# Kernel tuning notes

Measured on AMD Instinct MI355X. Metric: run time of the kernel, lower is better.

The kernel has to match this reference:

```python
import jax, jax.numpy as jnp
import numpy as np

B, N, OBS, H, A = 1024, 64, 128, 256, 16
NH = 4
HD = H // NH


def _linear_params(key, fan_in, fan_out):
    k1, k2 = jax.random.split(key)
    bound = 1.0 / np.sqrt(fan_in)
    W = jax.random.uniform(k1, (fan_out, fan_in), jnp.float32, -bound, bound)
    b = jax.random.uniform(k2, (fan_out,), jnp.float32, -bound, bound)
    return W, b


def setup_inputs() -> dict:
    key = jax.random.key(0)
    ks = jax.random.split(key, 10)
    obs = jax.random.normal(ks[0], (B, N, OBS), jnp.float32)
    adj = jax.random.randint(ks[1], (B, N, N), 0, 2).astype(jnp.float32)
    # guarantee every row has at least one neighbor (self-loop) so softmax is finite
    adj = jnp.maximum(adj, jnp.eye(N, dtype=jnp.float32)[None])
    W1, b1 = _linear_params(ks[2], OBS, H)
    W2, b2 = _linear_params(ks[3], H, H)
    Wq, bq = _linear_params(ks[4], H, H)
    Wk, bk = _linear_params(ks[5], H, H)
    Wv, bv = _linear_params(ks[6], H, H)
    Wo, bo = _linear_params(ks[7], H, H)
    Wc, bc = _linear_params(ks[8], H, H)
    W3, b3 = _linear_params(ks[9], H, A)
    return dict(obs=obs, adj=adj, W1=W1, b1=b1, W2=W2, b2=b2,
                Wq=Wq, bq=bq, Wk=Wk, bk=bk, Wv=Wv, bv=bv,
                Wo=Wo, bo=bo, Wc=Wc, bc=bc, W3=W3, b3=b3)


def reference(obs, adj, W1, b1, W2, b2, Wq, bq, Wk, bk, Wv, bv, Wo, bo, Wc, bc, W3, b3):
    lin = lambda x, W, b: jnp.einsum('bnd,od->bno', x, W) + b
    x = jax.nn.relu(lin(obs, W1, b1))
    x = jax.nn.relu(lin(x, W2, b2))
    # multi-head attention with adjacency mask
    def heads(t):  # [B,N,H] -> [B,NH,N,HD]
        return t.reshape(B, N, NH, HD).transpose(0, 2, 1, 3)
    q = heads(lin(x, Wq, bq))
    k = heads(lin(x, Wk, bk))
    v = heads(lin(x, Wv, bv))
    scores = jnp.einsum('bhqd,bhkd->bhqk', q, k) / np.sqrt(HD).astype(np.float32)
    scores = jnp.where(adj[:, None] == 0, -jnp.inf, scores)
    attn = jax.nn.softmax(scores, axis=-1)
    out = jnp.einsum('bhqk,bhkd->bhqd', attn, v)
    out = out.transpose(0, 2, 1, 3).reshape(B, N, H)
    x = lin(out, Wo, bo)
    # communication: adj @ fc(x)
    x = jnp.einsum('bnm,bmh->bnh', adj, lin(x, Wc, bc))
    return lin(x, W3, b3)
```

## Files before the change

### kernel.cpp

```cpp
#include <hip/hip_runtime.h>
#include <stdint.h>

typedef unsigned short u16;
typedef unsigned long long u64;
typedef __attribute__((ext_vector_type(8))) short short8;
typedef __attribute__((ext_vector_type(4))) float f32x4;

#define MFMA16 __builtin_amdgcn_mfma_f32_16x16x32_bf16

#define MTOT 65536

__device__ __forceinline__ u16 f2bf(float f) {
  union { float f; uint32_t u; } v; v.f = f;
  uint32_t r = v.u + 0x7FFFu + ((v.u >> 16) & 1u);
  return (u16)(r >> 16);
}

union U8 { short8 v; u16 u[8]; };
union U4 { u64 v; u16 u[4]; };

__device__ __forceinline__ void cp16(const void* g, void* l) {
  __builtin_amdgcn_global_load_lds(
      (const __attribute__((address_space(1))) void*)g,
      (__attribute__((address_space(3))) void*)l, 16, 0, 0);
}

__device__ __forceinline__ int swz(int row) { return ((row >> 1) & 3) << 4; }

__global__ __launch_bounds__(256) void k_l1(
    const float* __restrict__ Wc, const float* __restrict__ Wo,
    const float* __restrict__ bo, const float* __restrict__ bc,
    float* __restrict__ M1, float* __restrict__ bv,
    const float* __restrict__ W1, const float* __restrict__ W2,
    const float* __restrict__ Wq, const float* __restrict__ Wk,
    u16* o1, u16* o2, u16* oq, u16* ok) {
  const int bid = blockIdx.x, tid = threadIdx.x;
  if (bid < 256) {
    __shared__ float wcr[256];
    __shared__ float red[4];
    const int j = bid, d = tid;
    wcr[d] = Wc[j * 256 + d];
    __syncthreads();
    float acc = 0.f;
    for (int i = 0; i < 256; i++) acc += wcr[i] * Wo[i * 256 + d];
    M1[j * 256 + d] = acc;
    float p = wcr[d] * bo[d];
    for (int off = 32; off >= 1; off >>= 1) p += __shfl_xor(p, off);
    if ((d & 63) == 0) red[d >> 6] = p;
    __syncthreads();
    if (d == 0) bv[j] = bc[j] + red[0] + red[1] + red[2] + red[3];
  } else {
    int off8 = (bid - 256) * 256 + tid;
    const float* src; u16* dst;
    if      (off8 <  4096) { src = W1; dst = o1; }
    else if (off8 < 12288) { src = W2; dst = o2; off8 -= 4096; }
    else if (off8 < 20480) { src = Wq; dst = oq; off8 -= 12288; }
    else                   { src = Wk; dst = ok; off8 -= 20480; }
    const int e = off8 * 8;
    f32x4 a = *(const f32x4*)(src + e);
    f32x4 b = *(const f32x4*)(src + e + 4);
    U8 pk;
#pragma unroll
    for (int j = 0; j < 4; j++) { pk.u[j] = f2bf(a[j]); pk.u[4 + j] = f2bf(b[j]); }
    *(short8*)(dst + e) = pk.v;
  }
}

template<int K, bool AF32>
__device__ __forceinline__ void gemm_full2(
    const void* __restrict__ Ain, const u16* __restrict__ W,
    const float* __restrict__ bias, u16* __restrict__ C,
    const int m0, const bool relu, char* smem) {
  const int tid = threadIdx.x;
  const int lane = tid & 63, wid = tid >> 6;
  const int wr = wid >> 1, wc = wid & 1;
  const int ro = lane & 15, hi = lane >> 4;

  f32x4 acc0[4][4], acc1[4][4];
#pragma unroll
  for (int m = 0; m < 4; m++)
#pragma unroll
    for (int n = 0; n < 4; n++) {
      acc0[m][n] = (f32x4){0.f, 0.f, 0.f, 0.f};
      acc1[m][n] = (f32x4){0.f, 0.f, 0.f, 0.f};
    }

  auto stage = [&](int buf, int k0) {
    char* Ax = smem + buf * 24576;
    char* Bx = Ax + 8192;
    if (AF32) {
      const float* Af = (const float*)Ain;
#pragma unroll
      for (int it = 0; it < 2; it++) {
        const int e = (tid + it * 256) * 8;
        const int r = e >> 5, c = e & 31;
        const float* s = Af + (size_t)(m0 + r) * K + k0 + c;
        f32x4 a = *(const f32x4*)s, b = *(const f32x4*)(s + 4);
        U8 pk;
#pragma unroll
        for (int j = 0; j < 4; j++) { pk.u[j] = f2bf(a[j]); pk.u[4 + j] = f2bf(b[j]); }
        *(short8*)(Ax + ((r * 64 + c * 2) ^ swz(r))) = pk.v;
      }
    } else {
      const u16* Ab = (const u16*)Ain;
#pragma unroll
      for (int i = 0; i < 2; i++) {
        const int boff = i * 4096 + wid * 1024;
        const int t = boff + lane * 16;
        const int row = t >> 6;
        const int cb = (t & 63) ^ swz(row);
        cp16(Ab + (size_t)(m0 + row) * K + k0 + (cb >> 1), Ax + boff);
      }
    }
#pragma unroll
    for (int i = 0; i < 4; i++) {
      const int boff = i * 4096 + wid * 1024;
      const int t = boff + lane * 16;
      const int row = t >> 6;
      const int cb = (t & 63) ^ swz(row);
      cp16(W + (size_t)row * K + k0 + (cb >> 1), Bx + boff);
    }
  };

  auto compute = [&](int buf) {
    char* Ax = smem + buf * 24576;
    char* Bx = Ax + 8192;
    short8 af[4], fb0[4], fb1[4];
#pragma unroll
    for (int m = 0; m < 4; m++) {
      const int row = wr * 64 + m * 16 + ro;
      af[m] = *(const short8*)(Ax + ((row * 64 + hi * 16) ^ swz(row)));
    }
#pragma unroll
    for (int n = 0; n < 4; n++) {
      const int r0 = wc * 64 + n * 16 + ro;
      fb0[n] = *(const short8*)(Bx + ((r0 * 64 + hi * 16) ^ swz(r0)));
      const int r1 = 128 + r0;
      fb1[n] = *(const short8*)(Bx + ((r1 * 64 + hi * 16) ^ swz(r1)));
    }
    __builtin_amdgcn_s_setprio(1);
#pragma unroll
    for (int m = 0; m < 4; m++)
#pragma unroll
      for (int n = 0; n < 4; n++) {
        acc0[m][n] = MFMA16(af[m], fb0[n], acc0[m][n], 0, 0, 0);
        acc1[m][n] = MFMA16(af[m], fb1[n], acc1[m][n], 0, 0, 0);
      }
    __builtin_amdgcn_s_setprio(0);
  };

  constexpr int NT = K / 32;
  if (AF32) {
    stage(0, 0);
    __syncthreads();
    int cur = 0;
    for (int k0 = 32; k0 < K; k0 += 32) {
      stage(cur ^ 1, k0);
      compute(cur);
      __syncthreads();
      cur ^= 1;
    }
    compute(cur);
    __syncthreads();
  } else {
    stage(0, 0);
    stage(1, 32);
#pragma unroll
    for (int t = 0; t < NT; ++t) {
      if (t == NT - 1) asm volatile("s_waitcnt vmcnt(0)" ::: "memory");
      else             asm volatile("s_waitcnt vmcnt(6)" ::: "memory");
      asm volatile("s_barrier" ::: "memory");
      compute(t & 1);
      asm volatile("s_barrier" ::: "memory");
      if (t + 2 < NT) stage(t & 1, (t + 2) * 32);
    }
  }

  u16 (*Cs)[136] = (u16(*)[136])smem;
  auto ep = [&](f32x4 (&acc)[4][4], const int n0) {
#pragma unroll
    for (int half = 0; half < 2; half++) {
      if (wr == half) {
#pragma unroll
        for (int n = 0; n < 4; n++) {
          const int col = wc * 64 + n * 16 + ro;
          const float bb = bias[n0 + col];
#pragma unroll
          for (int m = 0; m < 4; m++)
#pragma unroll
            for (int j = 0; j < 4; j++) {
              float val = acc[m][n][j] + bb;
              if (relu) val = fmaxf(val, 0.f);
              Cs[m * 16 + hi * 4 + j][col] = f2bf(val);
            }
        }
      }
      __syncthreads();
      for (int i = tid; i < 64 * 16; i += 256) {
        const int r = i >> 4, c = (i & 15) << 3;
        *(short8*)(C + (size_t)(m0 + half * 64 + r) * 256 + n0 + c) = *(short8*)&Cs[r][c];
      }
      __syncthreads();
    }
  };
  ep(acc0, 0);
  ep(acc1, 128);
}

__global__ __launch_bounds__(256, 2) void k_gemm1_prep2(
    const float* __restrict__ obs, const u16* __restrict__ W1b,
    const float* __restrict__ b1, u16* __restrict__ x1,
    const float* __restrict__ W3, const float* __restrict__ M1,
    const float* __restrict__ bvchain, const float* __restrict__ bvw,
    float* __restrict__ Wzf, float* __restrict__ bz) {
  __shared__ char smem[49152];
  if (blockIdx.x < 512) {
    gemm_full2<128, true>(obs, W1b, b1, x1, (int)blockIdx.x * 128, true, smem);
    return;
  }
  float* w3r = (float*)smem;
  float* red = (float*)(smem + 1024);
  const int a = blockIdx.x - 512, d = threadIdx.x;
  w3r[d] = W3[a * 256 + d];
  __syncthreads();
  float acc = 0.f;
  for (int j = 0; j < 256; j++) acc += w3r[j] * M1[j * 256 + d];
  Wzf[a * 256 + d] = acc;
  float p = w3r[d] * bvchain[d] + acc * bvw[d];
  for (int off = 32; off >= 1; off >>= 1) p += __shfl_xor(p, off);
  if ((d & 63) == 0) red[d >> 6] = p;
  __syncthreads();
  if (d == 0) bz[a] = red[0] + red[1] + red[2] + red[3];
}

__global__ __launch_bounds__(256, 2) void k_x2_prep3(
    const u16* __restrict__ x1, const u16* __restrict__ W2b,
    const float* __restrict__ b2, u16* __restrict__ x2,
    const float* __restrict__ Wzf, const float* __restrict__ Wv,
    u16* __restrict__ G) {
  __shared__ char smem[49152];
  if (blockIdx.x < 512) {
    gemm_full2<256, false>(x1, W2b, b2, x2, (int)blockIdx.x * 128, true, smem);
    return;
  }
  const int g = blockIdx.x - 512, d2 = threadIdx.x;
  const int h = g >> 4, a = g & 15;
  float* wzr = (float*)smem;
  if (d2 < 64) wzr[d2] = Wzf[a * 256 + h * 64 + d2];
  __syncthreads();
  float acc = 0.f;
#pragma unroll 8
  for (int d = 0; d < 64; d++) acc += wzr[d] * Wv[(size_t)(h * 64 + d) * 256 + d2];
  G[g * 256 + d2] = f2bf(acc);
}

__global__ __launch_bounds__(256, 2) void k_qk_gemmv(
    const u16* __restrict__ x2,
    const u16* __restrict__ Wqb, const float* __restrict__ bq, u16* __restrict__ Qg,
    const u16* __restrict__ Wkb, const float* __restrict__ bk, u16* __restrict__ Kg,
    const u16* __restrict__ G, u16* __restrict__ Vzt) {
  __shared__ char smem[49152];
  const int bid = blockIdx.x;
  if (bid < 1024) {
    const int q = bid >> 4, r = bid & 15;
    const int mt = q * 8 + (r & 7);
    const int sub = r >> 3;
    gemm_full2<256, false>(x2, sub ? Wkb : Wqb, sub ? bk : bq, sub ? Kg : Qg,
                           mt * 128, false, smem);
    return;
  }
  const int tid = threadIdx.x;
  const int lane = tid & 63, w = tid >> 6;
  const int ro = lane & 15, hi = lane >> 4;
  const int m0 = (bid - 1024) * 128;

  f32x4 acc[2][4];
#pragma unroll
  for (int m = 0; m < 2; m++)
#pragma unroll
    for (int n = 0; n < 4; n++) acc[m][n] = (f32x4){0.f, 0.f, 0.f, 0.f};

  auto stage = [&](int buf, int k0) {
    char* Ax = smem + buf * 12288;
    char* Bx = Ax + 8192;
#pragma unroll
    for (int i = 0; i < 2; i++) {
      const int boff = i * 4096 + w * 1024;
      const int t = boff + lane * 16;
      const int row = t >> 6;
      const int cb = (t & 63) ^ swz(row);
      cp16(x2 + (size_t)(m0 + row) * 256 + k0 + (cb >> 1), Ax + boff);
    }
    {
      const int boff = w * 1024;
      const int t = boff + lane * 16;
      const int row = t >> 6;
      const int cb = (t & 63) ^ swz(row);
      cp16(G + (size_t)row * 256 + k0 + (cb >> 1), Bx + boff);
    }
  };
  auto compute = [&](int buf) {
    char* Ax = smem + buf * 12288;
    char* Bx = Ax + 8192;
    short8 af[2], fb[4];
#pragma unroll
    for (int m = 0; m < 2; m++) {
      const int row = w * 32 + m * 16 + ro;
      af[m] = *(const short8*)(Ax + ((row * 64 + hi * 16) ^ swz(row)));
    }
#pragma unroll
    for (int n = 0; n < 4; n++) {
      const int row = n * 16 + ro;
      fb[n] = *(const short8*)(Bx + ((row * 64 + hi * 16) ^ swz(row)));
    }
    __builtin_amdgcn_s_setprio(1);
#pragma unroll
    for (int m = 0; m < 2; m++)
#pragma unroll
      for (int n = 0; n < 4; n++)
        acc[m][n] = MFMA16(af[m], fb[n], acc[m][n], 0, 0, 0);
    __builtin_amdgcn_s_setprio(0);
  };

  stage(0, 0);
  stage(1, 32);
#pragma unroll
  for (int t = 0; t < 8; ++t) {
    if (t == 7) asm volatile("s_waitcnt vmcnt(0)" ::: "memory");
    else        asm volatile("s_waitcnt vmcnt(3)" ::: "memory");
    asm volatile("s_barrier" ::: "memory");
    compute(t & 1);
    asm volatile("s_barrier" ::: "memory");
    if (t + 2 < 8) stage(t & 1, (t + 2) * 32);
  }

#pragma unroll
  for (int m = 0; m < 2; m++) {
    const int rbase = w * 32 + m * 16;
    const int bidx = (m0 >> 6) + (rbase >> 6);
    const int ke = (rbase + hi * 4) & 63;
#pragma unroll
    for (int n = 0; n < 4; n++) {
      const int c = n * 16 + ro;
      U4 pk;
#pragma unroll
      for (int j = 0; j < 4; j++) pk.u[j] = f2bf(acc[m][n][j]);
      *(u64*)(Vzt + (size_t)bidx * 4096 + (size_t)c * 64 + ke) = pk.v;
    }
  }
}

__global__ __launch_bounds__(256, 2) void attn_fused(
    const u16* __restrict__ Qg, const u16* __restrict__ Kg,
    const u16* __restrict__ Vzt, const float* __restrict__ adj,
    const float* __restrict__ bz, const float* __restrict__ b3,
    float* __restrict__ out) {
  __shared__ u16 Ps[4][64][72];
  __shared__ float Zs[4][64][16];
  __shared__ u64 adjm[64];
  __shared__ u16 chunk[64][4];

  const int b = blockIdx.x, tid = threadIdx.x;
  const int lane = tid & 63, w = tid >> 6;
  const int ro = lane & 15, hi = lane >> 4;
  const int hc = w * 64;
  const size_t base = (size_t)b * 64 * 256;

  short8 kb[4][2];
#pragma unroll
  for (int n = 0; n < 4; n++)
#pragma unroll
    for (int ks = 0; ks < 2; ks++)
      kb[n][ks] = *(const short8*)(Kg + base + (size_t)(n * 16 + ro) * 256 + hc + ks * 32 + hi * 8);

  {
    const int q = tid >> 2, qa = tid & 3;
    const float* ar = adj + ((size_t)b * 64 + q) * 64 + qa * 16;
    f32x4 a0 = *(const f32x4*)(ar);
    f32x4 a1 = *(const f32x4*)(ar + 4);
    f32x4 a2 = *(const f32x4*)(ar + 8);
    f32x4 a3 = *(const f32x4*)(ar + 12);
    unsigned m16 = 0;
#pragma unroll
    for (int i = 0; i < 4; i++) {
      m16 |= (unsigned)(a0[i] != 0.f) << i;
      m16 |= (unsigned)(a1[i] != 0.f) << (4 + i);
      m16 |= (unsigned)(a2[i] != 0.f) << (8 + i);
      m16 |= (unsigned)(a3[i] != 0.f) << (12 + i);
    }
    chunk[q][qa] = (u16)m16;
  }

  f32x4 s[4][4];
#pragma unroll
  for (int m = 0; m < 4; m++) {
    short8 af[2];
#pragma unroll
    for (int ks = 0; ks < 2; ks++)
      af[ks] = *(const short8*)(Qg + base + (size_t)(m * 16 + ro) * 256 + hc + ks * 32 + hi * 8);
#pragma unroll
    for (int n = 0; n < 4; n++) s[m][n] = (f32x4){0.f, 0.f, 0.f, 0.f};
#pragma unroll
    for (int ks = 0; ks < 2; ks++)
#pragma unroll
      for (int n = 0; n < 4; n++)
        s[m][n] = MFMA16(af[ks], kb[n][ks], s[m][n], 0, 0, 0);
  }

  short8 vz[2];
#pragma unroll
  for (int ks = 0; ks < 2; ks++)
    vz[ks] = *(const short8*)(Vzt + (size_t)b * 4096 + (size_t)(hc / 4 + ro) * 64 + ks * 32 + hi * 8);

  __syncthreads();
  if (tid < 64)
    adjm[tid] = (u64)chunk[tid][0] | ((u64)chunk[tid][1] << 16) |
                ((u64)chunk[tid][2] << 32) | ((u64)chunk[tid][3] << 48);
  __syncthreads();

#pragma unroll
  for (int m = 0; m < 4; m++) {
#pragma unroll
    for (int j = 0; j < 4; j++) {
      const int q = m * 16 + hi * 4 + j;
      const u64 msk = adjm[q];
      float sv[4], ev[4];
      float mx = -3.0e38f;
#pragma unroll
      for (int n = 0; n < 4; n++) {
        const bool on = (msk >> (n * 16 + ro)) & 1ull;
        sv[n] = on ? s[m][n][j] * 0.125f : -3.0e38f;
        mx = fmaxf(mx, sv[n]);
      }
      mx = fmaxf(mx, __shfl_xor(mx, 1));
      mx = fmaxf(mx, __shfl_xor(mx, 2));
      mx = fmaxf(mx, __shfl_xor(mx, 4));
      mx = fmaxf(mx, __shfl_xor(mx, 8));
      float sum = 0.f;
#pragma unroll
      for (int n = 0; n < 4; n++) {
        ev[n] = (sv[n] > -1.0e37f) ? __expf(sv[n] - mx) : 0.f;
        sum += ev[n];
      }
      sum += __shfl_xor(sum, 1);
      sum += __shfl_xor(sum, 2);
      sum += __shfl_xor(sum, 4);
      sum += __shfl_xor(sum, 8);
      const float inv = 1.0f / sum;
#pragma unroll
      for (int n = 0; n < 4; n++)
        Ps[w][q][n * 16 + ro] = f2bf(ev[n] * inv);
    }
  }

#pragma unroll
  for (int m = 0; m < 4; m++) {
    short8 pa[2];
    pa[0] = *(const short8*)&Ps[w][m * 16 + ro][hi * 8];
    pa[1] = *(const short8*)&Ps[w][m * 16 + ro][32 + hi * 8];
    f32x4 oz = (f32x4){0.f, 0.f, 0.f, 0.f};
#pragma unroll
    for (int ks = 0; ks < 2; ks++)
      oz = MFMA16(pa[ks], vz[ks], oz, 0, 0, 0);
#pragma unroll
    for (int j = 0; j < 4; j++)
      Zs[w][m * 16 + hi * 4 + j][ro] = oz[j];
  }
  __syncthreads();

  for (int i = tid; i < 1024; i += 256) {
    const int r = i >> 4, a = i & 15;
    Zs[0][r][a] += Zs[1][r][a] + Zs[2][r][a] + Zs[3][r][a];
  }
  __syncthreads();

  {
    const int n = tid >> 2, a4 = (tid & 3) << 2;
    const u64 msk = adjm[n];
    const float deg = (float)__popcll(msk);
    float a0 = 0.f, a1 = 0.f, a2 = 0.f, a3 = 0.f;
#pragma unroll 8
    for (int m = 0; m < 64; m++) {
      const float wv = (float)((msk >> m) & 1ull);
      f32x4 z = *(const f32x4*)&Zs[0][m][a4];
      a0 += wv * z[0]; a1 += wv * z[1]; a2 += wv * z[2]; a3 += wv * z[3];
    }
    f32x4 r;
    r[0] = a0 + b3[a4 + 0] + deg * bz[a4 + 0];
    r[1] = a1 + b3[a4 + 1] + deg * bz[a4 + 1];
    r[2] = a2 + b3[a4 + 2] + deg * bz[a4 + 2];
    r[3] = a3 + b3[a4 + 3] + deg * bz[a4 + 3];
    *(f32x4*)(out + ((size_t)b * 64 + n) * 16 + a4) = r;
  }
}

extern "C" void kernel_launch(void* const* d_in, const int* in_sizes, int n_in,
                              void* d_out, int out_size, void* d_ws, size_t ws_size,
                              hipStream_t stream) {
  const float* obs = (const float*)d_in[0];
  const float* adj = (const float*)d_in[1];
  const float* W1  = (const float*)d_in[2];
  const float* b1  = (const float*)d_in[3];
  const float* W2  = (const float*)d_in[4];
  const float* b2  = (const float*)d_in[5];
  const float* Wq  = (const float*)d_in[6];
  const float* bq  = (const float*)d_in[7];
  const float* Wk  = (const float*)d_in[8];
  const float* bk  = (const float*)d_in[9];
  const float* Wv  = (const float*)d_in[10];
  const float* bvw = (const float*)d_in[11];
  const float* Wo  = (const float*)d_in[12];
  const float* bo  = (const float*)d_in[13];
  const float* Wc  = (const float*)d_in[14];
  const float* bc  = (const float*)d_in[15];
  const float* W3  = (const float*)d_in[16];
  const float* b3  = (const float*)d_in[17];
  float* out = (float*)d_out;

  char* ws = (char*)d_ws;
  const size_t BIG = (size_t)MTOT * 256 * 2;
  u16* buf0 = (u16*)(ws);
  u16* buf1 = (u16*)(ws + BIG);
  u16* buf2 = (u16*)(ws + 2 * BIG);
  u16* buf3 = (u16*)(ws + 3 * BIG);
  char* p = ws + 4 * BIG;
  u16* W1b = (u16*)p;              p += 128 * 256 * 2;
  u16* W2b = (u16*)p;              p += 256 * 256 * 2;
  u16* Wqb = (u16*)p;              p += 256 * 256 * 2;
  u16* Wkb = (u16*)p;              p += 256 * 256 * 2;
  float* M1 = (float*)p;           p += 256 * 256 * 4;
  float* Wzf = (float*)p;          p += 16 * 256 * 4;
  u16* G   = (u16*)p;              p += 64 * 256 * 2;
  float* bv = (float*)p;           p += 256 * 4;
  float* bz = (float*)p;           p += 16 * 4;

  dim3 blk(256);
  k_l1<<<dim3(368), blk, 0, stream>>>(Wc, Wo, bo, bc, M1, bv,
                                      W1, W2, Wq, Wk, W1b, W2b, Wqb, Wkb);
  k_gemm1_prep2<<<dim3(528), blk, 0, stream>>>(obs, W1b, b1, buf0,
                                               W3, M1, bv, bvw, Wzf, bz);
  k_x2_prep3<<<dim3(576), blk, 0, stream>>>(buf0, W2b, b2, buf1, Wzf, Wv, G);
  k_qk_gemmv<<<dim3(1536), blk, 0, stream>>>(buf1, Wqb, bq, buf2,
                                             Wkb, bk, buf3, G, buf0);
  attn_fused<<<dim3(1024), blk, 0, stream>>>(buf2, buf3, buf0, adj, bz, b3, out);
}
```

Measured before the change: 120.6 us.

## Precompute adjacency bitmasks in prep kernel and transpose GEMM tile for direct epilogue

Moves the adjacency-to-bitmask packing out of the attention kernel into extra blocks of the first weight-prep kernel, so the attention kernel loads 64 packed u64 masks per batch instead of 16 KB of float adjacency. It also swaps the MFMA operand roles in the shared GEMM helper so each lane holds 4 contiguous output columns. The epilogue then writes bias+relu bf16 results straight to global with 8-byte stores, dropping the LDS staging and its barriers. The cost is an extra global round-trip for the masks, more blocks in the prep kernel, and narrower, less coalesced output stores.

New measurement: 130.5 us. 8.2% more time.

```diff
diff --git a/kernel.cpp b/kernel.cpp
--- a/kernel.cpp
+++ b/kernel.cpp
@@ -33,7 +33,8 @@
     float* __restrict__ M1, float* __restrict__ bv,
     const float* __restrict__ W1, const float* __restrict__ W2,
     const float* __restrict__ Wq, const float* __restrict__ Wk,
-    u16* o1, u16* o2, u16* oq, u16* ok) {
+    u16* o1, u16* o2, u16* oq, u16* ok,
+    const float* __restrict__ adj, u64* __restrict__ adjm_g) {
   const int bid = blockIdx.x, tid = threadIdx.x;
   if (bid < 256) {
     __shared__ float wcr[256];
@@ -49,7 +50,7 @@
     if ((d & 63) == 0) red[d >> 6] = p;
     __syncthreads();
     if (d == 0) bv[j] = bc[j] + red[0] + red[1] + red[2] + red[3];
-  } else {
+  } else if (bid < 368) {
     int off8 = (bid - 256) * 256 + tid;
     const float* src; u16* dst;
     if      (off8 <  4096) { src = W1; dst = o1; }
@@ -63,6 +64,29 @@
 #pragma unroll
     for (int j = 0; j < 4; j++) { pk.u[j] = f2bf(a[j]); pk.u[4 + j] = f2bf(b[j]); }
     *(short8*)(dst + e) = pk.v;
+  } else {
+    __shared__ u16 chunk[64][4];
+    const int b = bid - 368;
+    const int q = tid >> 2, qa = tid & 3;
+    const float* ar = adj + ((size_t)b * 64 + q) * 64 + qa * 16;
+    f32x4 a0 = *(const f32x4*)(ar);
+    f32x4 a1 = *(const f32x4*)(ar + 4);
+    f32x4 a2 = *(const f32x4*)(ar + 8);
+    f32x4 a3 = *(const f32x4*)(ar + 12);
+    unsigned m16 = 0;
+#pragma unroll
+    for (int i = 0; i < 4; i++) {
+      m16 |= (unsigned)(a0[i] != 0.f) << i;
+      m16 |= (unsigned)(a1[i] != 0.f) << (4 + i);
+      m16 |= (unsigned)(a2[i] != 0.f) << (8 + i);
+      m16 |= (unsigned)(a3[i] != 0.f) << (12 + i);
+    }
+    chunk[q][qa] = (u16)m16;
+    __syncthreads();
+    if (tid < 64)
+      adjm_g[(size_t)b * 64 + tid] =
+          (u64)chunk[tid][0] | ((u64)chunk[tid][1] << 16) |
+          ((u64)chunk[tid][2] << 32) | ((u64)chunk[tid][3] << 48);
   }
 }
 
@@ -76,14 +100,11 @@
   const int wr = wid >> 1, wc = wid & 1;
   const int ro = lane & 15, hi = lane >> 4;
 
-  f32x4 acc0[4][4], acc1[4][4];
-#pragma unroll
-  for (int m = 0; m < 4; m++)
-#pragma unroll
-    for (int n = 0; n < 4; n++) {
-      acc0[m][n] = (f32x4){0.f, 0.f, 0.f, 0.f};
-      acc1[m][n] = (f32x4){0.f, 0.f, 0.f, 0.f};
-    }
+  f32x4 acc[8][4];
+#pragma unroll
+  for (int mw = 0; mw < 8; mw++)
+#pragma unroll
+    for (int nt = 0; nt < 4; nt++) acc[mw][nt] = (f32x4){0.f, 0.f, 0.f, 0.f};
 
   auto stage = [&](int buf, int k0) {
     char* Ax = smem + buf * 24576;
@@ -125,27 +146,21 @@
   auto compute = [&](int buf) {
     char* Ax = smem + buf * 24576;
     char* Bx = Ax + 8192;
-    short8 af[4], fb0[4], fb1[4];
-#pragma unroll
-    for (int m = 0; m < 4; m++) {
-      const int row = wr * 64 + m * 16 + ro;
-      af[m] = *(const short8*)(Ax + ((row * 64 + hi * 16) ^ swz(row)));
-    }
-#pragma unroll
-    for (int n = 0; n < 4; n++) {
-      const int r0 = wc * 64 + n * 16 + ro;
-      fb0[n] = *(const short8*)(Bx + ((r0 * 64 + hi * 16) ^ swz(r0)));
-      const int r1 = 128 + r0;
-      fb1[n] = *(const short8*)(Bx + ((r1 * 64 + hi * 16) ^ swz(r1)));
+    short8 fb[4];
+#pragma unroll
+    for (int nt = 0; nt < 4; nt++) {
+      const int row = wr * 64 + nt * 16 + ro;
+      fb[nt] = *(const short8*)(Ax + ((row * 64 + hi * 16) ^ swz(row)));
     }
     __builtin_amdgcn_s_setprio(1);
 #pragma unroll
-    for (int m = 0; m < 4; m++)
-#pragma unroll
-      for (int n = 0; n < 4; n++) {
-        acc0[m][n] = MFMA16(af[m], fb0[n], acc0[m][n], 0, 0, 0);
-        acc1[m][n] = MFMA16(af[m], fb1[n], acc1[m][n], 0, 0, 0);
-      }
+    for (int mw = 0; mw < 8; mw++) {
+      const int row = wc * 128 + mw * 16 + ro;
+      short8 af = *(const short8*)(Bx + ((row * 64 + hi * 16) ^ swz(row)));
+#pragma unroll
+      for (int nt = 0; nt < 4; nt++)
+        acc[mw][nt] = MFMA16(af, fb[nt], acc[mw][nt], 0, 0, 0);
+    }
     __builtin_amdgcn_s_setprio(0);
   };
 
@@ -161,7 +176,6 @@
       cur ^= 1;
     }
     compute(cur);
-    __syncthreads();
   } else {
     stage(0, 0);
     stage(1, 32);
@@ -176,35 +190,23 @@
     }
   }
 
-  u16 (*Cs)[136] = (u16(*)[136])smem;
-  auto ep = [&](f32x4 (&acc)[4][4], const int n0) {
-#pragma unroll
-    for (int half = 0; half < 2; half++) {
-      if (wr == half) {
-#pragma unroll
-        for (int n = 0; n < 4; n++) {
-          const int col = wc * 64 + n * 16 + ro;
-          const float bb = bias[n0 + col];
-#pragma unroll
-          for (int m = 0; m < 4; m++)
-#pragma unroll
-            for (int j = 0; j < 4; j++) {
-              float val = acc[m][n][j] + bb;
-              if (relu) val = fmaxf(val, 0.f);
-              Cs[m * 16 + hi * 4 + j][col] = f2bf(val);
-            }
-        }
+#pragma unroll
+  for (int mw = 0; mw < 8; mw++) {
+    const int col = wc * 128 + mw * 16 + hi * 4;
+    f32x4 bb = *(const f32x4*)(bias + col);
+#pragma unroll
+    for (int nt = 0; nt < 4; nt++) {
+      const int tok = m0 + wr * 64 + nt * 16 + ro;
+      U4 pk;
+#pragma unroll
+      for (int j = 0; j < 4; j++) {
+        float val = acc[mw][nt][j] + bb[j];
+        if (relu) val = fmaxf(val, 0.f);
+        pk.u[j] = f2bf(val);
       }
-      __syncthreads();
-      for (int i = tid; i < 64 * 16; i += 256) {
-        const int r = i >> 4, c = (i & 15) << 3;
-        *(short8*)(C + (size_t)(m0 + half * 64 + r) * 256 + n0 + c) = *(short8*)&Cs[r][c];
-      }
-      __syncthreads();
-    }
-  };
-  ep(acc0, 0);
-  ep(acc1, 128);
+      *(u64*)(C + (size_t)tok * 256 + col) = pk.v;
+    }
+  }
 }
 
 __global__ __launch_bounds__(256, 2) void k_gemm1_prep2(
@@ -352,13 +354,12 @@
 
 __global__ __launch_bounds__(256, 2) void attn_fused(
     const u16* __restrict__ Qg, const u16* __restrict__ Kg,
-    const u16* __restrict__ Vzt, const float* __restrict__ adj,
+    const u16* __restrict__ Vzt, const u64* __restrict__ adjm_g,
     const float* __restrict__ bz, const float* __restrict__ b3,
     float* __restrict__ out) {
   __shared__ u16 Ps[4][64][72];
   __shared__ float Zs[4][64][16];
   __shared__ u64 adjm[64];
-  __shared__ u16 chunk[64][4];
 
   const int b = blockIdx.x, tid = threadIdx.x;
   const int lane = tid & 63, w = tid >> 6;
@@ -366,6 +367,8 @@
   const int hc = w * 64;
   const size_t base = (size_t)b * 64 * 256;
 
+  if (tid < 64) adjm[tid] = adjm_g[(size_t)b * 64 + tid];
+
   short8 kb[4][2];
 #pragma unroll
   for (int n = 0; n < 4; n++)
@@ -373,24 +376,6 @@
     for (int ks = 0; ks < 2; ks++)
       kb[n][ks] = *(const short8*)(Kg + base + (size_t)(n * 16 + ro) * 256 + hc + ks * 32 + hi * 8);
 
-  {
-    const int q = tid >> 2, qa = tid & 3;
-    const float* ar = adj + ((size_t)b * 64 + q) * 64 + qa * 16;
-    f32x4 a0 = *(const f32x4*)(ar);
-    f32x4 a1 = *(const f32x4*)(ar + 4);
-    f32x4 a2 = *(const f32x4*)(ar + 8);
-    f32x4 a3 = *(const f32x4*)(ar + 12);
-    unsigned m16 = 0;
-#pragma unroll
-    for (int i = 0; i < 4; i++) {
-      m16 |= (unsigned)(a0[i] != 0.f) << i;
-      m16 |= (unsigned)(a1[i] != 0.f) << (4 + i);
-      m16 |= (unsigned)(a2[i] != 0.f) << (8 + i);
-      m16 |= (unsigned)(a3[i] != 0.f) << (12 + i);
-    }
-    chunk[q][qa] = (u16)m16;
-  }
-
   f32x4 s[4][4];
 #pragma unroll
   for (int m = 0; m < 4; m++) {
@@ -412,10 +397,6 @@
   for (int ks = 0; ks < 2; ks++)
     vz[ks] = *(const short8*)(Vzt + (size_t)b * 4096 + (size_t)(hc / 4 + ro) * 64 + ks * 32 + hi * 8);
 
-  __syncthreads();
-  if (tid < 64)
-    adjm[tid] = (u64)chunk[tid][0] | ((u64)chunk[tid][1] << 16) |
-                ((u64)chunk[tid][2] << 32) | ((u64)chunk[tid][3] << 48);
   __syncthreads();
 
 #pragma unroll
@@ -533,14 +514,16 @@
   u16* G   = (u16*)p;              p += 64 * 256 * 2;
   float* bv = (float*)p;           p += 256 * 4;
   float* bz = (float*)p;           p += 16 * 4;
+  u64* adjm_g = (u64*)p;           p += (size_t)MTOT * 8;
 
   dim3 blk(256);
-  k_l1<<<dim3(368), blk, 0, stream>>>(Wc, Wo, bo, bc, M1, bv,
-                                      W1, W2, Wq, Wk, W1b, W2b, Wqb, Wkb);
+  k_l1<<<dim3(1392), blk, 0, stream>>>(Wc, Wo, bo, bc, M1, bv,
+                                       W1, W2, Wq, Wk, W1b, W2b, Wqb, Wkb,
+                                       adj, adjm_g);
   k_gemm1_prep2<<<dim3(528), blk, 0, stream>>>(obs, W1b, b1, buf0,
                                                W3, M1, bv, bvw, Wzf, bz);
   k_x2_prep3<<<dim3(576), blk, 0, stream>>>(buf0, W2b, b2, buf1, Wzf, Wv, G);
   k_qk_gemmv<<<dim3(1536), blk, 0, stream>>>(buf1, Wqb, bq, buf2,
                                              Wkb, bk, buf3, G, buf0);
-  attn_fused<<<dim3(1024), blk, 0, stream>>>(buf2, buf3, buf0, adj, bz, b3, out);
-}
+  attn_fused<<<dim3(1024), blk, 0, stream>>>(buf2, buf3, buf0, adjm_g, bz, b3, out);
+}
```

## Process two M-tiles per block in QK/V GEMMs and precompute adjacency bitmasks

Applied to the files above, without the earlier changes.

The Q/K GEMM blocks now each process two 128-row M-tiles across a 16-step pipelined loop, with a new LDS-staged epilogue. The V projection blocks likewise cover two M-tiles, which halves the block count from 1536 to 768 and shrinks per-block pipeline prologue overhead. Adjacency-to-bitmask conversion moves out of the attention kernel into 1024 extra blocks of the first kernel, so attention reads a compact u64 mask instead of the float adjacency matrix. In exchange, shared memory per block grows to 66.5KB, which may limit occupancy, and there is an extra global round trip for the mask.

Result: slower. 151.4 us (+25.5%).

```diff
diff --git a/kernel.cpp b/kernel.cpp
--- a/kernel.cpp
+++ b/kernel.cpp
@@ -33,7 +33,8 @@
     float* __restrict__ M1, float* __restrict__ bv,
     const float* __restrict__ W1, const float* __restrict__ W2,
     const float* __restrict__ Wq, const float* __restrict__ Wk,
-    u16* o1, u16* o2, u16* oq, u16* ok) {
+    u16* o1, u16* o2, u16* oq, u16* ok,
+    const float* __restrict__ adj, u64* __restrict__ adjm_g) {
   const int bid = blockIdx.x, tid = threadIdx.x;
   if (bid < 256) {
     __shared__ float wcr[256];
@@ -49,7 +50,7 @@
     if ((d & 63) == 0) red[d >> 6] = p;
     __syncthreads();
     if (d == 0) bv[j] = bc[j] + red[0] + red[1] + red[2] + red[3];
-  } else {
+  } else if (bid < 368) {
     int off8 = (bid - 256) * 256 + tid;
     const float* src; u16* dst;
     if      (off8 <  4096) { src = W1; dst = o1; }
@@ -63,6 +64,29 @@
 #pragma unroll
     for (int j = 0; j < 4; j++) { pk.u[j] = f2bf(a[j]); pk.u[4 + j] = f2bf(b[j]); }
     *(short8*)(dst + e) = pk.v;
+  } else {
+    __shared__ u16 chunk[64][4];
+    const int b = bid - 368;
+    const int q = tid >> 2, qa = tid & 3;
+    const float* ar = adj + ((size_t)b * 64 + q) * 64 + qa * 16;
+    f32x4 a0 = *(const f32x4*)(ar);
+    f32x4 a1 = *(const f32x4*)(ar + 4);
+    f32x4 a2 = *(const f32x4*)(ar + 8);
+    f32x4 a3 = *(const f32x4*)(ar + 12);
+    unsigned m16 = 0;
+#pragma unroll
+    for (int i = 0; i < 4; i++) {
+      m16 |= (unsigned)(a0[i] != 0.f) << i;
+      m16 |= (unsigned)(a1[i] != 0.f) << (4 + i);
+      m16 |= (unsigned)(a2[i] != 0.f) << (8 + i);
+      m16 |= (unsigned)(a3[i] != 0.f) << (12 + i);
+    }
+    chunk[q][qa] = (u16)m16;
+    __syncthreads();
+    if (tid < 64)
+      adjm_g[(size_t)b * 64 + tid] =
+          (u64)chunk[tid][0] | ((u64)chunk[tid][1] << 16) |
+          ((u64)chunk[tid][2] << 32) | ((u64)chunk[tid][3] << 48);
   }
 }
 
@@ -259,20 +283,138 @@
     const u16* __restrict__ Wqb, const float* __restrict__ bq, u16* __restrict__ Qg,
     const u16* __restrict__ Wkb, const float* __restrict__ bk, u16* __restrict__ Kg,
     const u16* __restrict__ G, u16* __restrict__ Vzt) {
-  __shared__ char smem[49152];
+  __shared__ char smem[66560];
   const int bid = blockIdx.x;
-  if (bid < 1024) {
+  const int tid = threadIdx.x;
+  const int lane = tid & 63, wid = tid >> 6;
+  const int ro = lane & 15, hi = lane >> 4;
+
+  if (bid < 512) {
     const int q = bid >> 4, r = bid & 15;
-    const int mt = q * 8 + (r & 7);
+    const int mtp = q * 8 + (r & 7);
     const int sub = r >> 3;
-    gemm_full2<256, false>(x2, sub ? Wkb : Wqb, sub ? bk : bq, sub ? Kg : Qg,
-                           mt * 128, false, smem);
+    const u16* W = sub ? Wkb : Wqb;
+    const float* bias = sub ? bk : bq;
+    u16* C = sub ? Kg : Qg;
+    const int m_base = mtp * 256;
+    const int wr = wid >> 1, wc = wid & 1;
+
+    f32x4 acc0[4][4], acc1[4][4];
+#pragma unroll
+    for (int m = 0; m < 4; m++)
+#pragma unroll
+      for (int n = 0; n < 4; n++) {
+        acc0[m][n] = (f32x4){0.f, 0.f, 0.f, 0.f};
+        acc1[m][n] = (f32x4){0.f, 0.f, 0.f, 0.f};
+      }
+
+    auto stage = [&](int g) {
+      const int m0 = m_base + (g >> 3) * 128;
+      const int k0 = (g & 7) * 32;
+      char* Ax = smem + (g & 1) * 24576;
+      char* Bx = Ax + 8192;
+#pragma unroll
+      for (int i = 0; i < 2; i++) {
+        const int boff = i * 4096 + wid * 1024;
+        const int t = boff + lane * 16;
+        const int row = t >> 6;
+        const int cb = (t & 63) ^ swz(row);
+        cp16(x2 + (size_t)(m0 + row) * 256 + k0 + (cb >> 1), Ax + boff);
+      }
+#pragma unroll
+      for (int i = 0; i < 4; i++) {
+        const int boff = i * 4096 + wid * 1024;
+        const int t = boff + lane * 16;
+        const int row = t >> 6;
+        const int cb = (t & 63) ^ swz(row);
+        cp16(W + (size_t)row * 256 + k0 + (cb >> 1), Bx + boff);
+      }
+    };
+    auto compute = [&](int buf) {
+      char* Ax = smem + buf * 24576;
+      char* Bx = Ax + 8192;
+      short8 af[4], fb0[4], fb1[4];
+#pragma unroll
+      for (int m = 0; m < 4; m++) {
+        const int row = wr * 64 + m * 16 + ro;
+        af[m] = *(const short8*)(Ax + ((row * 64 + hi * 16) ^ swz(row)));
+      }
+#pragma unroll
+      for (int n = 0; n < 4; n++) {
+        const int r0 = wc * 64 + n * 16 + ro;
+        fb0[n] = *(const short8*)(Bx + ((r0 * 64 + hi * 16) ^ swz(r0)));
+        const int r1 = 128 + r0;
+        fb1[n] = *(const short8*)(Bx + ((r1 * 64 + hi * 16) ^ swz(r1)));
+      }
+      __builtin_amdgcn_s_setprio(1);
+#pragma unroll
+      for (int m = 0; m < 4; m++)
+#pragma unroll
+        for (int n = 0; n < 4; n++) {
+          acc0[m][n] = MFMA16(af[m], fb0[n], acc0[m][n], 0, 0, 0);
+          acc1[m][n] = MFMA16(af[m], fb1[n], acc1[m][n], 0, 0, 0);
+        }
+      __builtin_amdgcn_s_setprio(0);
+    };
+    u16 (*Cs)[136] = (u16(*)[136])(smem + 49152);
+    auto ep = [&](f32x4 (&acc)[4][4], const int n0, const int m0) {
+#pragma unroll
+      for (int half = 0; half < 2; half++) {
+        if (wr == half) {
+#pragma unroll
+          for (int n = 0; n < 4; n++) {
+            const int col = wc * 64 + n * 16 + ro;
+            const float bb = bias[n0 + col];
+#pragma unroll
+            for (int m = 0; m < 4; m++)
+#pragma unroll
+              for (int j = 0; j < 4; j++)
+                Cs[m * 16 + hi * 4 + j][col] = f2bf(acc[m][n][j] + bb);
+          }
+        }
+        asm volatile("s_waitcnt lgkmcnt(0)" ::: "memory");
+        __builtin_amdgcn_sched_barrier(0);
+        __builtin_amdgcn_s_barrier();
+        for (int i = tid; i < 64 * 16; i += 256) {
+          const int r = i >> 4, c = (i & 15) << 3;
+          *(short8*)(C + (size_t)(m0 + half * 64 + r) * 256 + n0 + c) = *(short8*)&Cs[r][c];
+        }
+        asm volatile("s_waitcnt lgkmcnt(0)" ::: "memory");
+        __builtin_amdgcn_sched_barrier(0);
+        __builtin_amdgcn_s_barrier();
+      }
+    };
+
+    stage(0);
+    stage(1);
+#pragma unroll
+    for (int g = 0; g < 16; ++g) {
+      if (g == 15) asm volatile("s_waitcnt vmcnt(0)" ::: "memory");
+      else         asm volatile("s_waitcnt vmcnt(6)" ::: "memory");
+      asm volatile("s_barrier" ::: "memory");
+      compute(g & 1);
+      asm volatile("s_barrier" ::: "memory");
+      if (g + 2 < 16) stage(g + 2);
+      if ((g & 7) == 7) {
+        const int m0 = m_base + (g >> 3) * 128;
+        ep(acc0, 0, m0);
+        ep(acc1, 128, m0);
+        if (g == 7) {
+#pragma unroll
+          for (int m = 0; m < 4; m++)
+#pragma unroll
+            for (int n = 0; n < 4; n++) {
+              acc0[m][n] = (f32x4){0.f, 0.f, 0.f, 0.f};
+              acc1[m][n] = (f32x4){0.f, 0.f, 0.f, 0.f};
+            }
+        }
+      }
+    }
     return;
   }
-  const int tid = threadIdx.x;
-  const int lane = tid & 63, w = tid >> 6;
-  const int ro = lane & 15, hi = lane >> 4;
-  const int m0 = (bid - 1024) * 128;
+
+  const int w = wid;
+  const int m_base = (bid - 512) * 256;
 
   f32x4 acc[2][4];
 #pragma unroll
@@ -280,8 +422,10 @@
 #pragma unroll
     for (int n = 0; n < 4; n++) acc[m][n] = (f32x4){0.f, 0.f, 0.f, 0.f};
 
-  auto stage = [&](int buf, int k0) {
-    char* Ax = smem + buf * 12288;
+  auto stage = [&](int g) {
+    const int m0 = m_base + (g >> 3) * 128;
+    const int k0 = (g & 7) * 32;
+    char* Ax = smem + (g & 1) * 12288;
     char* Bx = Ax + 8192;
 #pragma unroll
     for (int i = 0; i < 2; i++) {
@@ -321,44 +465,53 @@
         acc[m][n] = MFMA16(af[m], fb[n], acc[m][n], 0, 0, 0);
     __builtin_amdgcn_s_setprio(0);
   };
-
-  stage(0, 0);
-  stage(1, 32);
-#pragma unroll
-  for (int t = 0; t < 8; ++t) {
-    if (t == 7) asm volatile("s_waitcnt vmcnt(0)" ::: "memory");
-    else        asm volatile("s_waitcnt vmcnt(3)" ::: "memory");
+  auto ep = [&](const int m0) {
+#pragma unroll
+    for (int m = 0; m < 2; m++) {
+      const int rbase = w * 32 + m * 16;
+      const int bidx = (m0 >> 6) + (rbase >> 6);
+      const int ke = (rbase + hi * 4) & 63;
+#pragma unroll
+      for (int n = 0; n < 4; n++) {
+        const int c = n * 16 + ro;
+        U4 pk;
+#pragma unroll
+        for (int j = 0; j < 4; j++) pk.u[j] = f2bf(acc[m][n][j]);
+        *(u64*)(Vzt + (size_t)bidx * 4096 + (size_t)c * 64 + ke) = pk.v;
+      }
+    }
+  };
+
+  stage(0);
+  stage(1);
+#pragma unroll
+  for (int g = 0; g < 16; ++g) {
+    if (g == 15) asm volatile("s_waitcnt vmcnt(0)" ::: "memory");
+    else         asm volatile("s_waitcnt vmcnt(3)" ::: "memory");
     asm volatile("s_barrier" ::: "memory");
-    compute(t & 1);
+    compute(g & 1);
     asm volatile("s_barrier" ::: "memory");
-    if (t + 2 < 8) stage(t & 1, (t + 2) * 32);
-  }
-
-#pragma unroll
-  for (int m = 0; m < 2; m++) {
-    const int rbase = w * 32 + m * 16;
-    const int bidx = (m0 >> 6) + (rbase >> 6);
-    const int ke = (rbase + hi * 4) & 63;
-#pragma unroll
-    for (int n = 0; n < 4; n++) {
-      const int c = n * 16 + ro;
-      U4 pk;
-#pragma unroll
-      for (int j = 0; j < 4; j++) pk.u[j] = f2bf(acc[m][n][j]);
-      *(u64*)(Vzt + (size_t)bidx * 4096 + (size_t)c * 64 + ke) = pk.v;
+    if (g + 2 < 16) stage(g + 2);
+    if ((g & 7) == 7) {
+      ep(m_base + (g >> 3) * 128);
+      if (g == 7) {
+#pragma unroll
+        for (int m = 0; m < 2; m++)
+#pragma unroll
+          for (int n = 0; n < 4; n++) acc[m][n] = (f32x4){0.f, 0.f, 0.f, 0.f};
+      }
     }
   }
 }
 
 __global__ __launch_bounds__(256, 2) void attn_fused(
     const u16* __restrict__ Qg, const u16* __restrict__ Kg,
-    const u16* __restrict__ Vzt, const float* __restrict__ adj,
+    const u16* __restrict__ Vzt, const u64* __restrict__ adjm_g,
     const float* __restrict__ bz, const float* __restrict__ b3,
     float* __restrict__ out) {
   __shared__ u16 Ps[4][64][72];
   __shared__ float Zs[4][64][16];
   __shared__ u64 adjm[64];
-  __shared__ u16 chunk[64][4];
 
   const int b = blockIdx.x, tid = threadIdx.x;
   const int lane = tid & 63, w = tid >> 6;
@@ -366,6 +519,8 @@
   const int hc = w * 64;
   const size_t base = (size_t)b * 64 * 256;
 
+  if (tid < 64) adjm[tid] = adjm_g[(size_t)b * 64 + tid];
+
   short8 kb[4][2];
 #pragma unroll
   for (int n = 0; n < 4; n++)
@@ -373,24 +528,6 @@
     for (int ks = 0; ks < 2; ks++)
       kb[n][ks] = *(const short8*)(Kg + base + (size_t)(n * 16 + ro) * 256 + hc + ks * 32 + hi * 8);
 
-  {
-    const int q = tid >> 2, qa = tid & 3;
-    const float* ar = adj + ((size_t)b * 64 + q) * 64 + qa * 16;
-    f32x4 a0 = *(const f32x4*)(ar);
-    f32x4 a1 = *(const f32x4*)(ar + 4);
-    f32x4 a2 = *(const f32x4*)(ar + 8);
-    f32x4 a3 = *(const f32x4*)(ar + 12);
-    unsigned m16 = 0;
-#pragma unroll
-    for (int i = 0; i < 4; i++) {
-      m16 |= (unsigned)(a0[i] != 0.f) << i;
-      m16 |= (unsigned)(a1[i] != 0.f) << (4 + i);
-      m16 |= (unsigned)(a2[i] != 0.f) << (8 + i);
-      m16 |= (unsigned)(a3[i] != 0.f) << (12 + i);
-    }
-    chunk[q][qa] = (u16)m16;
-  }
-
   f32x4 s[4][4];
 #pragma unroll
   for (int m = 0; m < 4; m++) {
@@ -412,10 +549,6 @@
   for (int ks = 0; ks < 2; ks++)
     vz[ks] = *(const short8*)(Vzt + (size_t)b * 4096 + (size_t)(hc / 4 + ro) * 64 + ks * 32 + hi * 8);
 
-  __syncthreads();
-  if (tid < 64)
-    adjm[tid] = (u64)chunk[tid][0] | ((u64)chunk[tid][1] << 16) |
-                ((u64)chunk[tid][2] << 32) | ((u64)chunk[tid][3] << 48);
   __syncthreads();
 
 #pragma unroll
@@ -533,14 +666,16 @@
   u16* G   = (u16*)p;              p += 64 * 256 * 2;
   float* bv = (float*)p;           p += 256 * 4;
   float* bz = (float*)p;           p += 16 * 4;
+  u64* adjm_g = (u64*)p;           p += (size_t)MTOT * 8;
 
   dim3 blk(256);
-  k_l1<<<dim3(368), blk, 0, stream>>>(Wc, Wo, bo, bc, M1, bv,
-                                      W1, W2, Wq, Wk, W1b, W2b, Wqb, Wkb);
+  k_l1<<<dim3(1392), blk, 0, stream>>>(Wc, Wo, bo, bc, M1, bv,
+                                       W1, W2, Wq, Wk, W1b, W2b, Wqb, Wkb,
+                                       adj, adjm_g);
   k_gemm1_prep2<<<dim3(528), blk, 0, stream>>>(obs, W1b, b1, buf0,
                                                W3, M1, bv, bvw, Wzf, bz);
   k_x2_prep3<<<dim3(576), blk, 0, stream>>>(buf0, W2b, b2, buf1, Wzf, Wv, G);
-  k_qk_gemmv<<<dim3(1536), blk, 0, stream>>>(buf1, Wqb, bq, buf2,
-                                             Wkb, bk, buf3, G, buf0);
-  attn_fused<<<dim3(1024), blk, 0, stream>>>(buf2, buf3, buf0, adj, bz, b3, out);
-}
+  k_qk_gemmv<<<dim3(768), blk, 0, stream>>>(buf1, Wqb, bq, buf2,
+                                            Wkb, bk, buf3, G, buf0);
+  attn_fused<<<dim3(1024), blk, 0, stream>>>(buf2, buf3, buf0, adjm_g, bz, b3, out);
+}
```
